# Kernel tuning notes

Measured on AMD Instinct MI355X. Metric: run time of the kernel, lower is better.

Reference implementation:

```python
import jax, jax.numpy as jnp
import numpy as np

N = 40000      # nodes
E = 640000     # edges
G = 2048       # graphs
D = 128        # emb_dim
T = 10         # num_tasks
L = 5          # layers
ATOM_VOCAB = 64
BOND_VOCAB = 8
BN_EPS = 1e-5


def _bn(x, g, b, m, v):
    # inference-mode BatchNorm1d with running stats
    return (x - m) * jax.lax.rsqrt(v + BN_EPS) * g + b


def setup_inputs() -> dict:
    key = jax.random.key(0)
    ks = jax.random.split(key, 24)
    inp = {
        "x_atom": jax.random.randint(ks[0], (N, 9), 0, ATOM_VOCAB),
        "edge_index": jax.random.randint(ks[1], (2, E), 0, N),
        "edge_attr": jax.random.randint(ks[2], (E, 3), 0, BOND_VOCAB),
        "batch": jnp.sort(jax.random.randint(ks[3], (N,), 0, G)),
        # embedding tables
        "atom_emb": jax.random.normal(ks[4], (9, ATOM_VOCAB, D)) * 0.1,
        "bond_emb": jax.random.normal(ks[5], (L, 3, BOND_VOCAB, D)) * 0.1,
        # per-layer GIN params (stacked over L)
        "eps": jnp.zeros((L,)),
        "W1": jax.random.normal(ks[6], (L, D, 2 * D)) * 0.05,
        "b1": jnp.zeros((L, 2 * D)),
        "g1": jnp.ones((L, 2 * D)),
        "bt1": jnp.zeros((L, 2 * D)),
        "m1": jax.random.normal(ks[7], (L, 2 * D)) * 0.1,
        "v1": jax.random.uniform(ks[8], (L, 2 * D), minval=0.5, maxval=1.5),
        "W2": jax.random.normal(ks[9], (L, 2 * D, D)) * 0.05,
        "b2": jnp.zeros((L, D)),
        # outer BatchNorm per layer
        "gO": jnp.ones((L, D)),
        "btO": jnp.zeros((L, D)),
        "mO": jax.random.normal(ks[10], (L, D)) * 0.1,
        "vO": jax.random.uniform(ks[11], (L, D), minval=0.5, maxval=1.5),
        # prediction head
        "Wp": jax.random.normal(ks[12], (D, T)) * 0.05,
        "bp": jnp.zeros((T,)),
    }
    return inp


def reference(x_atom, edge_index, edge_attr, batch, atom_emb, bond_emb, eps,
              W1, b1, g1, bt1, m1, v1, W2, b2, gO, btO, mO, vO, Wp, bp):
    src, dst = edge_index[0], edge_index[1]
    # AtomEncoder: sum of per-feature embeddings -> [N, D]
    x = atom_emb[jnp.arange(9)[None, :], x_atom].sum(axis=1)
    feat3 = jnp.arange(3)[None, :]
    for i in range(L):
        # BondEncoder for this layer -> [E, D]
        e = bond_emb[i][feat3, edge_attr].sum(axis=1)
        # message: relu(x_j + edge_emb); aggregate: scatter-add at dst
        msg = jax.nn.relu(x[src] + e)
        agg = jax.ops.segment_sum(msg, dst, num_segments=N)
        h = (1.0 + eps[i]) * x + agg
        # MLP: Linear -> BN -> ReLU -> Linear
        h = jax.nn.relu(_bn(h @ W1[i] + b1[i], g1[i], bt1[i], m1[i], v1[i]))
        h = h @ W2[i] + b2[i]
        # outer BN; ReLU after all but last layer (dropout = identity in eval)
        x = _bn(h, gO[i], btO[i], mO[i], vO[i])
        if i < L - 1:
            x = jax.nn.relu(x)
    # global mean pool over graphs
    sums = jax.ops.segment_sum(x, batch, num_segments=G)
    cnt = jax.ops.segment_sum(jnp.ones((N,), x.dtype), batch, num_segments=G)
    pooled = sums / jnp.maximum(cnt, 1.0)[:, None]
    return pooled @ Wp + bp
```

## Files before the change

kernel.cpp:

```cpp
#include <hip/hip_runtime.h>
#include <hip/hip_bf16.h>

#define NN 40000
#define NE 640000
#define NG 2048
#define DD 128
#define NT 10
#define NL 5
#define NB 80

typedef __attribute__((ext_vector_type(8))) short short8;
typedef __attribute__((ext_vector_type(4))) float f32x4;
typedef unsigned short ushort_t;

static __device__ __forceinline__ ushort_t f2b(float f) {
    return __bfloat16_as_ushort(__float2bfloat16(f));
}
static __device__ __forceinline__ float b2f(ushort_t u) {
    return __bfloat162float(__ushort_as_bfloat16(u));
}

__global__ void __launch_bounds__(256)
k_setup(const float* __restrict__ W1, const float* __restrict__ W2,
        const float* __restrict__ bemb, const int* __restrict__ xa,
        const float* __restrict__ aemb, const int* __restrict__ ei,
        ushort_t* __restrict__ W1P, ushort_t* __restrict__ W2P,
        ushort_t* __restrict__ ebsum16, ushort_t* __restrict__ x16,
        int* __restrict__ deg) {
    int b = blockIdx.x, t = threadIdx.x;
    if (b < 1280) {
        int tid = b * 256 + t;
        int layer = tid >> 16;
        int r = tid & 65535;
        int half = r >> 15;
        int q = r & 32767;
        int j = q & 7;
        int lane = (q >> 3) & 63;
        if (half == 0) {
            int kk = (q >> 9) & 3;
            int nt = q >> 11;
            int n = nt * 16 + (lane & 15);
            int k = kk * 32 + (lane >> 4) * 8 + j;
            W1P[layer * 32768 + q] = f2b(W1[(layer * DD + k) * 256 + n]);
        } else {
            int kk = (q >> 9) & 7;
            int nt = q >> 12;
            int n = nt * 16 + (lane & 15);
            int k = kk * 32 + (lane >> 4) * 8 + j;
            W2P[layer * 32768 + q] = f2b(W2[(layer * 256 + k) * DD + n]);
        }
        int d = tid & 127;
        int c = (tid >> 7) & 511;
        const float* bl = bemb + (size_t)layer * 3 * 8 * DD;
        ebsum16[tid] = f2b(bl[(c & 7) * DD + d] + bl[(8 + ((c >> 3) & 7)) * DD + d] +
                           bl[(16 + (c >> 6)) * DD + d]);
    } else if (b < 21280) {
        int half = t >> 7, d = t & 127;
        int n = (b - 1280) * 2 + half;
        __shared__ int idx[2][9];
        if (d < 9) idx[half][d] = xa[n * 9 + d];
        __syncthreads();
        float s = 0.f;
#pragma unroll
        for (int f = 0; f < 9; ++f) s += aemb[(f * 64 + idx[half][f]) * DD + d];
        x16[n * DD + d] = f2b(s);
    } else {
        int e = (b - 21280) * 256 + t;
        atomicAdd(&deg[ei[NE + e]], 1);
    }
}


__global__ void k_scan1(const int* __restrict__ deg, int* __restrict__ off,
                        int* __restrict__ blksum) {
    int b = blockIdx.x, t = threadIdx.x;
    int i = b * 256 + t;
    __shared__ int s[256];
    int v = (i < NN) ? deg[i] : 0;
    s[t] = v;
    __syncthreads();
    for (int d = 1; d < 256; d <<= 1) {
        int add = (t >= d) ? s[t - d] : 0;
        __syncthreads();
        s[t] += add;
        __syncthreads();
    }
    if (i <= NN) off[i] = s[t] - v;
    if (t == 255) blksum[b] = s[255];
}

__global__ void k_scan2(int* __restrict__ blk) {
    int t = threadIdx.x;
    __shared__ int s[256];
    int v = blk[t];
    s[t] = v;
    __syncthreads();
    for (int d = 1; d < 256; d <<= 1) {
        int add = (t >= d) ? s[t - d] : 0;
        __syncthreads();
        s[t] += add;
        __syncthreads();
    }
    blk[256 + t] = s[t] - v;
}

__global__ void k_scan3(int* __restrict__ off, const int* __restrict__ blk) {
    int b = blockIdx.x, t = threadIdx.x;
    int i = b * 256 + t;
    if (i <= NN) off[i] += blk[256 + b];
}

__global__ void __launch_bounds__(256)
k_bucket(const int* __restrict__ ei, const int* __restrict__ ea,
         const int* __restrict__ off, int* __restrict__ gbk,
         int2* __restrict__ ebuf) {
    __shared__ int hist[NB];
    __shared__ int sbase[NB];
    int t = threadIdx.x;
    int e0 = blockIdx.x * 1024;
    if (t < NB) hist[t] = 0;
    __syncthreads();
    int rank[4], buck[4], rec[4], dstv[4];
#pragma unroll
    for (int k = 0; k < 4; ++k) {
        int e = e0 + k * 256 + t;
        int src = ei[e];
        int dst = ei[NE + e];
        int a0 = ea[e * 3 + 0], a1 = ea[e * 3 + 1], a2 = ea[e * 3 + 2];
        rec[k] = src | ((a0 | (a1 << 3) | (a2 << 6)) << 16);
        dstv[k] = dst;
        int b = dst >> 9;
        buck[k] = b;
        rank[k] = atomicAdd(&hist[b], 1);
    }
    __syncthreads();
    if (t < NB) sbase[t] = atomicAdd(&gbk[t], hist[t]);
    __syncthreads();
#pragma unroll
    for (int k = 0; k < 4; ++k) {
        int b = buck[k];
        int slot = off[b << 9] + sbase[b] + rank[k];
        ebuf[slot] = make_int2(rec[k], dstv[k]);
    }
}

__global__ void k_scatter2(const int2* __restrict__ ebuf, const int* __restrict__ off,
                           int* __restrict__ cursor, int2* __restrict__ epack) {
    int i = blockIdx.x * 256 + threadIdx.x;
    int2 s = ebuf[i];
    int dst = s.y;
    int p = off[dst] + atomicAdd(&cursor[dst], 1);
    epack[p] = make_int2(s.x & 0xFFFF, s.x >> 16);
}

__global__ void __launch_bounds__(128)
k_gather(const ushort_t* __restrict__ xin, const int* __restrict__ off,
         const int2* __restrict__ epack, const ushort_t* __restrict__ ebsum16,
         const float* __restrict__ eps, int layer, ushort_t* __restrict__ h16) {
    int t = threadIdx.x;
    int lane = t & 63;
    int n = blockIdx.x * 2 + (t >> 6);
    const ushort2* x2 = (const ushort2*)xin;
    const ushort2* eb2 = (const ushort2*)ebsum16;
    ushort2 xv = x2[n * 64 + lane];
    float es = 1.f + eps[layer];
    float ax = es * b2f(xv.x), ay = es * b2f(xv.y);
    int p = off[n], p1 = off[n + 1];

    int2 e0, e1, e2, e3;
    bool have = (p + 4 <= p1);
    if (have) { e0 = epack[p]; e1 = epack[p + 1]; e2 = epack[p + 2]; e3 = epack[p + 3]; }
    while (have) {
        int np = p + 4;
        bool nh = (np + 4 <= p1);
        int2 f0, f1, f2, f3;
        if (nh) { f0 = epack[np]; f1 = epack[np + 1]; f2 = epack[np + 2]; f3 = epack[np + 3]; }
        ushort2 v0 = eb2[e0.y * 64 + lane];
        ushort2 s0 = x2[e0.x * 64 + lane];
        ushort2 v1 = eb2[e1.y * 64 + lane];
        ushort2 s1 = x2[e1.x * 64 + lane];
        ushort2 v2 = eb2[e2.y * 64 + lane];
        ushort2 s2 = x2[e2.x * 64 + lane];
        ushort2 v3 = eb2[e3.y * 64 + lane];
        ushort2 s3 = x2[e3.x * 64 + lane];
        ax += fmaxf(b2f(v0.x) + b2f(s0.x), 0.f) + fmaxf(b2f(v1.x) + b2f(s1.x), 0.f) +
              fmaxf(b2f(v2.x) + b2f(s2.x), 0.f) + fmaxf(b2f(v3.x) + b2f(s3.x), 0.f);
        ay += fmaxf(b2f(v0.y) + b2f(s0.y), 0.f) + fmaxf(b2f(v1.y) + b2f(s1.y), 0.f) +
              fmaxf(b2f(v2.y) + b2f(s2.y), 0.f) + fmaxf(b2f(v3.y) + b2f(s3.y), 0.f);
        p = np;
        e0 = f0; e1 = f1; e2 = f2; e3 = f3;
        have = nh;
    }
    for (; p < p1; ++p) {
        int2 er = epack[p];
        ushort2 ev = eb2[er.y * 64 + lane];
        ushort2 sv = x2[er.x * 64 + lane];
        ax += fmaxf(b2f(ev.x) + b2f(sv.x), 0.f);
        ay += fmaxf(b2f(ev.y) + b2f(sv.y), 0.f);
    }
    ushort2 o;
    o.x = f2b(ax);
    o.y = f2b(ay);
    ((ushort2*)h16)[n * 64 + lane] = o;
}

__global__ void __launch_bounds__(256)
k_mlp_mfma(const ushort_t* __restrict__ h16, const ushort_t* __restrict__ W1P,
           const ushort_t* __restrict__ W2P, const float* __restrict__ b1,
           const float* __restrict__ g1, const float* __restrict__ bt1,
           const float* __restrict__ m1, const float* __restrict__ v1,
           const float* __restrict__ b2_, const float* __restrict__ gO,
           const float* __restrict__ btO, const float* __restrict__ mO,
           const float* __restrict__ vO, int relu, ushort_t* __restrict__ xout) {
    __shared__ ushort_t aS[32 * 136];
    __shared__ ushort_t mid[32 * 264];
    int t = threadIdx.x;
    int wave = t >> 6, lane = t & 63;
    int row0 = blockIdx.x * 32;
    int lrow = lane & 15, quad = lane >> 4;

#pragma unroll
    for (int ps = 0; ps < 2; ++ps) {
        int idx = ps * 256 + t;
        int r = idx >> 4, c = (idx & 15) * 8;
        *(short8*)&aS[r * 136 + c] = *(const short8*)&h16[(row0 + r) * DD + c];
    }
    __syncthreads();

    f32x4 acc1[2][4];
#pragma unroll
    for (int rt = 0; rt < 2; ++rt)
#pragma unroll
        for (int i = 0; i < 4; ++i) acc1[rt][i] = (f32x4){0.f, 0.f, 0.f, 0.f};
#pragma unroll
    for (int kk = 0; kk < 4; ++kk) {
        short8 af0 = *(const short8*)&aS[lrow * 136 + kk * 32 + quad * 8];
        short8 af1 = *(const short8*)&aS[(16 + lrow) * 136 + kk * 32 + quad * 8];
#pragma unroll
        for (int i = 0; i < 4; ++i) {
            int nt = wave * 4 + i;
            short8 bf = *(const short8*)&W1P[((nt * 4 + kk) * 64 + lane) * 8];
            acc1[0][i] = __builtin_amdgcn_mfma_f32_16x16x32_bf16(af0, bf, acc1[0][i], 0, 0, 0);
            acc1[1][i] = __builtin_amdgcn_mfma_f32_16x16x32_bf16(af1, bf, acc1[1][i], 0, 0, 0);
        }
    }
#pragma unroll
    for (int i = 0; i < 4; ++i) {
        int col = (wave * 4 + i) * 16 + lrow;
        float s1 = g1[col] * rsqrtf(v1[col] + 1e-5f);
        float sh = bt1[col] - (m1[col] - b1[col]) * s1;
#pragma unroll
        for (int rt = 0; rt < 2; ++rt)
#pragma unroll
            for (int r = 0; r < 4; ++r) {
                int row = rt * 16 + quad * 4 + r;
                float o = acc1[rt][i][r] * s1 + sh;
                mid[row * 264 + col] = f2b(fmaxf(o, 0.f));
            }
    }
    __syncthreads();

    f32x4 acc2[2][2];
#pragma unroll
    for (int rt = 0; rt < 2; ++rt)
#pragma unroll
        for (int i = 0; i < 2; ++i) acc2[rt][i] = (f32x4){0.f, 0.f, 0.f, 0.f};
#pragma unroll
    for (int kk = 0; kk < 8; ++kk) {
        short8 af0 = *(const short8*)&mid[lrow * 264 + kk * 32 + quad * 8];
        short8 af1 = *(const short8*)&mid[(16 + lrow) * 264 + kk * 32 + quad * 8];
#pragma unroll
        for (int i = 0; i < 2; ++i) {
            int nt = wave * 2 + i;
            short8 bf = *(const short8*)&W2P[((nt * 8 + kk) * 64 + lane) * 8];
            acc2[0][i] = __builtin_amdgcn_mfma_f32_16x16x32_bf16(af0, bf, acc2[0][i], 0, 0, 0);
            acc2[1][i] = __builtin_amdgcn_mfma_f32_16x16x32_bf16(af1, bf, acc2[1][i], 0, 0, 0);
        }
    }
#pragma unroll
    for (int i = 0; i < 2; ++i) {
        int col = (wave * 2 + i) * 16 + lrow;
        float s = gO[col] * rsqrtf(vO[col] + 1e-5f);
        float sh = btO[col] - (mO[col] - b2_[col]) * s;
#pragma unroll
        for (int rt = 0; rt < 2; ++rt)
#pragma unroll
            for (int r = 0; r < 4; ++r) {
                int row = rt * 16 + quad * 4 + r;
                float o = acc2[rt][i][r] * s + sh;
                if (relu) o = fmaxf(o, 0.f);
                xout[(row0 + row) * DD + col] = f2b(o);
            }
    }
}

__global__ void k_poolhead(const ushort_t* __restrict__ x16,
                           const int* __restrict__ batch,
                           const float* __restrict__ Wp, const float* __restrict__ bp,
                           float* __restrict__ out) {
    int g = blockIdx.x, d = threadIdx.x;
    int lo = 0, hi = NN;
    while (lo < hi) { int m = (lo + hi) >> 1; if (batch[m] < g) lo = m + 1; else hi = m; }
    int start = lo;
    hi = NN;
    while (lo < hi) { int m = (lo + hi) >> 1; if (batch[m] < g + 1) lo = m + 1; else hi = m; }
    int end = lo;
    float s = 0.f;
    for (int n = start; n < end; ++n) s += b2f(x16[n * DD + d]);
    float c = fmaxf((float)(end - start), 1.f);
    __shared__ float p[DD];
    p[d] = s / c;
    __syncthreads();
    if (d < NT) {
        float acc = bp[d];
#pragma unroll 8
        for (int k = 0; k < DD; ++k) acc = fmaf(p[k], Wp[k * NT + d], acc);
        out[g * NT + d] = acc;
    }
}

extern "C" void kernel_launch(void* const* d_in, const int* in_sizes, int n_in,
                              void* d_out, int out_size, void* d_ws, size_t ws_size,
                              hipStream_t stream) {
    const int* x_atom = (const int*)d_in[0];
    const int* edge_index = (const int*)d_in[1];
    const int* edge_attr = (const int*)d_in[2];
    const int* batch = (const int*)d_in[3];
    const float* atom_emb = (const float*)d_in[4];
    const float* bond_emb = (const float*)d_in[5];
    const float* eps = (const float*)d_in[6];
    const float* W1 = (const float*)d_in[7];
    const float* b1 = (const float*)d_in[8];
    const float* g1 = (const float*)d_in[9];
    const float* bt1 = (const float*)d_in[10];
    const float* m1 = (const float*)d_in[11];
    const float* v1 = (const float*)d_in[12];
    const float* W2 = (const float*)d_in[13];
    const float* b2 = (const float*)d_in[14];
    const float* gO = (const float*)d_in[15];
    const float* btO = (const float*)d_in[16];
    const float* mO = (const float*)d_in[17];
    const float* vO = (const float*)d_in[18];
    const float* Wp = (const float*)d_in[19];
    const float* bp = (const float*)d_in[20];

    ushort_t* x16a = (ushort_t*)d_ws;
    ushort_t* x16b = x16a + NN * DD;
    ushort_t* h16 = x16b + NN * DD;
    ushort_t* W1P = h16 + NN * DD;
    ushort_t* W2P = W1P + NL * 32768;
    ushort_t* ebsum16 = W2P + NL * 32768;
    int* deg = (int*)(ebsum16 + NL * 65536);
    int* off = deg + NN;
    int* blk = off + 40064;
    int* cursor = blk + 512;
    int* gbk = cursor + NN;
    int2* epack = (int2*)(gbk + 128);
    int2* ebuf = epack + NE;

    hipMemsetAsync(deg, 0, (NN + 40064 + 512 + NN + 128) * sizeof(int), stream);

    k_setup<<<23780, 256, 0, stream>>>(W1, W2, bond_emb, x_atom, atom_emb,
                                       edge_index, W1P, W2P, ebsum16, x16a, deg);
    k_scan1<<<157, 256, 0, stream>>>(deg, off, blk);
    k_scan2<<<1, 256, 0, stream>>>(blk);
    k_scan3<<<157, 256, 0, stream>>>(off, blk);
    k_bucket<<<NE / 1024, 256, 0, stream>>>(edge_index, edge_attr, off, gbk, ebuf);
    k_scatter2<<<NE / 256, 256, 0, stream>>>(ebuf, off, cursor, epack);

    for (int i = 0; i < NL; ++i) {
        ushort_t* xin = (i & 1) ? x16b : x16a;
        ushort_t* xout = (i & 1) ? x16a : x16b;
        k_gather<<<NN / 2, 128, 0, stream>>>(xin, off, epack, ebsum16 + i * 65536,
                                             eps, i, h16);
        k_mlp_mfma<<<NN / 32, 256, 0, stream>>>(
            h16, W1P + (size_t)i * 32768, W2P + (size_t)i * 32768, b1 + i * 256,
            g1 + i * 256, bt1 + i * 256, m1 + i * 256, v1 + i * 256, b2 + i * DD,
            gO + i * DD, btO + i * DD, mO + i * DD, vO + i * DD,
            (i < NL - 1) ? 1 : 0, xout);
    }
    k_poolhead<<<NG, DD, 0, stream>>>(x16b, batch, Wp, bp, (float*)d_out);
}
```

Measured before the change: 426.5 us.

## Fuse neighbor gather into MLP kernel with 512-thread blocks

Merges the per-layer gather kernel and the MFMA MLP kernel into one kernel. Each 512-thread block aggregates its 32 nodes straight into shared memory, then runs the two GEMMs, with work split across 8 waves instead of 4. This removes the h16 round trip through global memory and one launch per layer. In exchange, the latency-bound gather now runs at a block granularity of 32 nodes per block, which may reduce latency hiding, and the MFMA phase waits on the slowest node in the block.

```diff
diff --git a/kernel.cpp b/kernel.cpp
--- a/kernel.cpp
+++ b/kernel.cpp
@@ -153,100 +153,95 @@
     epack[p] = make_int2(s.x & 0xFFFF, s.x >> 16);
 }
 
-__global__ void __launch_bounds__(128)
-k_gather(const ushort_t* __restrict__ xin, const int* __restrict__ off,
-         const int2* __restrict__ epack, const ushort_t* __restrict__ ebsum16,
-         const float* __restrict__ eps, int layer, ushort_t* __restrict__ h16) {
-    int t = threadIdx.x;
-    int lane = t & 63;
-    int n = blockIdx.x * 2 + (t >> 6);
-    const ushort2* x2 = (const ushort2*)xin;
-    const ushort2* eb2 = (const ushort2*)ebsum16;
-    ushort2 xv = x2[n * 64 + lane];
-    float es = 1.f + eps[layer];
-    float ax = es * b2f(xv.x), ay = es * b2f(xv.y);
-    int p = off[n], p1 = off[n + 1];
-
-    int2 e0, e1, e2, e3;
-    bool have = (p + 4 <= p1);
-    if (have) { e0 = epack[p]; e1 = epack[p + 1]; e2 = epack[p + 2]; e3 = epack[p + 3]; }
-    while (have) {
-        int np = p + 4;
-        bool nh = (np + 4 <= p1);
-        int2 f0, f1, f2, f3;
-        if (nh) { f0 = epack[np]; f1 = epack[np + 1]; f2 = epack[np + 2]; f3 = epack[np + 3]; }
-        ushort2 v0 = eb2[e0.y * 64 + lane];
-        ushort2 s0 = x2[e0.x * 64 + lane];
-        ushort2 v1 = eb2[e1.y * 64 + lane];
-        ushort2 s1 = x2[e1.x * 64 + lane];
-        ushort2 v2 = eb2[e2.y * 64 + lane];
-        ushort2 s2 = x2[e2.x * 64 + lane];
-        ushort2 v3 = eb2[e3.y * 64 + lane];
-        ushort2 s3 = x2[e3.x * 64 + lane];
-        ax += fmaxf(b2f(v0.x) + b2f(s0.x), 0.f) + fmaxf(b2f(v1.x) + b2f(s1.x), 0.f) +
-              fmaxf(b2f(v2.x) + b2f(s2.x), 0.f) + fmaxf(b2f(v3.x) + b2f(s3.x), 0.f);
-        ay += fmaxf(b2f(v0.y) + b2f(s0.y), 0.f) + fmaxf(b2f(v1.y) + b2f(s1.y), 0.f) +
-              fmaxf(b2f(v2.y) + b2f(s2.y), 0.f) + fmaxf(b2f(v3.y) + b2f(s3.y), 0.f);
-        p = np;
-        e0 = f0; e1 = f1; e2 = f2; e3 = f3;
-        have = nh;
-    }
-    for (; p < p1; ++p) {
-        int2 er = epack[p];
-        ushort2 ev = eb2[er.y * 64 + lane];
-        ushort2 sv = x2[er.x * 64 + lane];
-        ax += fmaxf(b2f(ev.x) + b2f(sv.x), 0.f);
-        ay += fmaxf(b2f(ev.y) + b2f(sv.y), 0.f);
-    }
-    ushort2 o;
-    o.x = f2b(ax);
-    o.y = f2b(ay);
-    ((ushort2*)h16)[n * 64 + lane] = o;
-}
-
-__global__ void __launch_bounds__(256)
-k_mlp_mfma(const ushort_t* __restrict__ h16, const ushort_t* __restrict__ W1P,
-           const ushort_t* __restrict__ W2P, const float* __restrict__ b1,
-           const float* __restrict__ g1, const float* __restrict__ bt1,
-           const float* __restrict__ m1, const float* __restrict__ v1,
-           const float* __restrict__ b2_, const float* __restrict__ gO,
-           const float* __restrict__ btO, const float* __restrict__ mO,
-           const float* __restrict__ vO, int relu, ushort_t* __restrict__ xout) {
+__global__ void __launch_bounds__(512)
+k_layer(const ushort_t* __restrict__ xin, const int* __restrict__ off,
+        const int2* __restrict__ epack, const ushort_t* __restrict__ ebsum16,
+        const float* __restrict__ eps, int layer,
+        const ushort_t* __restrict__ W1P, const ushort_t* __restrict__ W2P,
+        const float* __restrict__ b1, const float* __restrict__ g1,
+        const float* __restrict__ bt1, const float* __restrict__ m1,
+        const float* __restrict__ v1, const float* __restrict__ b2_,
+        const float* __restrict__ gO, const float* __restrict__ btO,
+        const float* __restrict__ mO, const float* __restrict__ vO, int relu,
+        ushort_t* __restrict__ xout) {
     __shared__ ushort_t aS[32 * 136];
     __shared__ ushort_t mid[32 * 264];
     int t = threadIdx.x;
     int wave = t >> 6, lane = t & 63;
     int row0 = blockIdx.x * 32;
+
+    {
+        const ushort2* x2 = (const ushort2*)xin;
+        const ushort2* eb2 = (const ushort2*)ebsum16;
+        float es = 1.f + eps[layer];
+#pragma unroll
+        for (int i = 0; i < 4; ++i) {
+            int lr = wave * 4 + i;
+            int n = row0 + lr;
+            ushort2 xv = x2[n * 64 + lane];
+            float ax = es * b2f(xv.x), ay = es * b2f(xv.y);
+            int p = off[n], p1 = off[n + 1];
+            int2 e0, e1, e2, e3;
+            bool have = (p + 4 <= p1);
+            if (have) { e0 = epack[p]; e1 = epack[p + 1]; e2 = epack[p + 2]; e3 = epack[p + 3]; }
+            while (have) {
+                int np = p + 4;
+                bool nh = (np + 4 <= p1);
+                int2 f0, f1, f2, f3;
+                if (nh) { f0 = epack[np]; f1 = epack[np + 1]; f2 = epack[np + 2]; f3 = epack[np + 3]; }
+                ushort2 v0 = eb2[e0.y * 64 + lane];
+                ushort2 s0 = x2[e0.x * 64 + lane];
+                ushort2 v1v = eb2[e1.y * 64 + lane];
+                ushort2 s1 = x2[e1.x * 64 + lane];
+                ushort2 v2 = eb2[e2.y * 64 + lane];
+                ushort2 s2 = x2[e2.x * 64 + lane];
+                ushort2 v3 = eb2[e3.y * 64 + lane];
+                ushort2 s3 = x2[e3.x * 64 + lane];
+                ax += fmaxf(b2f(v0.x) + b2f(s0.x), 0.f) + fmaxf(b2f(v1v.x) + b2f(s1.x), 0.f) +
+                      fmaxf(b2f(v2.x) + b2f(s2.x), 0.f) + fmaxf(b2f(v3.x) + b2f(s3.x), 0.f);
+                ay += fmaxf(b2f(v0.y) + b2f(s0.y), 0.f) + fmaxf(b2f(v1v.y) + b2f(s1.y), 0.f) +
+                      fmaxf(b2f(v2.y) + b2f(s2.y), 0.f) + fmaxf(b2f(v3.y) + b2f(s3.y), 0.f);
+                p = np;
+                e0 = f0; e1 = f1; e2 = f2; e3 = f3;
+                have = nh;
+            }
+            for (; p < p1; ++p) {
+                int2 er = epack[p];
+                ushort2 ev = eb2[er.y * 64 + lane];
+                ushort2 sv = x2[er.x * 64 + lane];
+                ax += fmaxf(b2f(ev.x) + b2f(sv.x), 0.f);
+                ay += fmaxf(b2f(ev.y) + b2f(sv.y), 0.f);
+            }
+            ushort2 o;
+            o.x = f2b(ax);
+            o.y = f2b(ay);
+            *(ushort2*)&aS[lr * 136 + lane * 2] = o;
+        }
+    }
+    __syncthreads();
+
     int lrow = lane & 15, quad = lane >> 4;
 
-#pragma unroll
-    for (int ps = 0; ps < 2; ++ps) {
-        int idx = ps * 256 + t;
-        int r = idx >> 4, c = (idx & 15) * 8;
-        *(short8*)&aS[r * 136 + c] = *(const short8*)&h16[(row0 + r) * DD + c];
-    }
-    __syncthreads();
-
-    f32x4 acc1[2][4];
+    f32x4 acc1[2][2];
 #pragma unroll
     for (int rt = 0; rt < 2; ++rt)
 #pragma unroll
-        for (int i = 0; i < 4; ++i) acc1[rt][i] = (f32x4){0.f, 0.f, 0.f, 0.f};
+        for (int i = 0; i < 2; ++i) acc1[rt][i] = (f32x4){0.f, 0.f, 0.f, 0.f};
 #pragma unroll
     for (int kk = 0; kk < 4; ++kk) {
         short8 af0 = *(const short8*)&aS[lrow * 136 + kk * 32 + quad * 8];
         short8 af1 = *(const short8*)&aS[(16 + lrow) * 136 + kk * 32 + quad * 8];
 #pragma unroll
-        for (int i = 0; i < 4; ++i) {
-            int nt = wave * 4 + i;
+        for (int i = 0; i < 2; ++i) {
+            int nt = wave * 2 + i;
             short8 bf = *(const short8*)&W1P[((nt * 4 + kk) * 64 + lane) * 8];
             acc1[0][i] = __builtin_amdgcn_mfma_f32_16x16x32_bf16(af0, bf, acc1[0][i], 0, 0, 0);
             acc1[1][i] = __builtin_amdgcn_mfma_f32_16x16x32_bf16(af1, bf, acc1[1][i], 0, 0, 0);
         }
     }
 #pragma unroll
-    for (int i = 0; i < 4; ++i) {
-        int col = (wave * 4 + i) * 16 + lrow;
+    for (int i = 0; i < 2; ++i) {
+        int col = (wave * 2 + i) * 16 + lrow;
         float s1 = g1[col] * rsqrtf(v1[col] + 1e-5f);
         float sh = bt1[col] - (m1[col] - b1[col]) * s1;
 #pragma unroll
@@ -260,26 +255,19 @@
     }
     __syncthreads();
 
-    f32x4 acc2[2][2];
-#pragma unroll
-    for (int rt = 0; rt < 2; ++rt)
-#pragma unroll
-        for (int i = 0; i < 2; ++i) acc2[rt][i] = (f32x4){0.f, 0.f, 0.f, 0.f};
+    f32x4 acc2[2];
+#pragma unroll
+    for (int rt = 0; rt < 2; ++rt) acc2[rt] = (f32x4){0.f, 0.f, 0.f, 0.f};
 #pragma unroll
     for (int kk = 0; kk < 8; ++kk) {
         short8 af0 = *(const short8*)&mid[lrow * 264 + kk * 32 + quad * 8];
         short8 af1 = *(const short8*)&mid[(16 + lrow) * 264 + kk * 32 + quad * 8];
-#pragma unroll
-        for (int i = 0; i < 2; ++i) {
-            int nt = wave * 2 + i;
-            short8 bf = *(const short8*)&W2P[((nt * 8 + kk) * 64 + lane) * 8];
-            acc2[0][i] = __builtin_amdgcn_mfma_f32_16x16x32_bf16(af0, bf, acc2[0][i], 0, 0, 0);
-            acc2[1][i] = __builtin_amdgcn_mfma_f32_16x16x32_bf16(af1, bf, acc2[1][i], 0, 0, 0);
-        }
-    }
-#pragma unroll
-    for (int i = 0; i < 2; ++i) {
-        int col = (wave * 2 + i) * 16 + lrow;
+        short8 bf = *(const short8*)&W2P[((wave * 8 + kk) * 64 + lane) * 8];
+        acc2[0] = __builtin_amdgcn_mfma_f32_16x16x32_bf16(af0, bf, acc2[0], 0, 0, 0);
+        acc2[1] = __builtin_amdgcn_mfma_f32_16x16x32_bf16(af1, bf, acc2[1], 0, 0, 0);
+    }
+    {
+        int col = wave * 16 + lrow;
         float s = gO[col] * rsqrtf(vO[col] + 1e-5f);
         float sh = btO[col] - (mO[col] - b2_[col]) * s;
 #pragma unroll
@@ -287,7 +275,7 @@
 #pragma unroll
             for (int r = 0; r < 4; ++r) {
                 int row = rt * 16 + quad * 4 + r;
-                float o = acc2[rt][i][r] * s + sh;
+                float o = acc2[rt][r] * s + sh;
                 if (relu) o = fmaxf(o, 0.f);
                 xout[(row0 + row) * DD + col] = f2b(o);
             }
@@ -346,8 +334,7 @@
 
     ushort_t* x16a = (ushort_t*)d_ws;
     ushort_t* x16b = x16a + NN * DD;
-    ushort_t* h16 = x16b + NN * DD;
-    ushort_t* W1P = h16 + NN * DD;
+    ushort_t* W1P = x16b + NN * DD;
     ushort_t* W2P = W1P + NL * 32768;
     ushort_t* ebsum16 = W2P + NL * 32768;
     int* deg = (int*)(ebsum16 + NL * 65536);
@@ -371,10 +358,9 @@
     for (int i = 0; i < NL; ++i) {
         ushort_t* xin = (i & 1) ? x16b : x16a;
         ushort_t* xout = (i & 1) ? x16a : x16b;
-        k_gather<<<NN / 2, 128, 0, stream>>>(xin, off, epack, ebsum16 + i * 65536,
-                                             eps, i, h16);
-        k_mlp_mfma<<<NN / 32, 256, 0, stream>>>(
-            h16, W1P + (size_t)i * 32768, W2P + (size_t)i * 32768, b1 + i * 256,
+        k_layer<<<NN / 32, 512, 0, stream>>>(
+            xin, off, epack, ebsum16 + i * 65536, eps, i,
+            W1P + (size_t)i * 32768, W2P + (size_t)i * 32768, b1 + i * 256,
             g1 + i * 256, bt1 + i * 256, m1 + i * 256, v1 + i * 256, b2 + i * DD,
             gO + i * DD, btO + i * DD, mO + i * DD, vO + i * DD,
             (i < NL - 1) ? 1 : 0, xout);
```

Result: slower. 438.0 us (+2.7%).
